# Kernel tuning notes

Measured on AMD Instinct MI355X. Metric: run time of the kernel, lower is better.

Reference implementation:

```python
import jax, jax.numpy as jnp
import numpy as np

L, H, C, DH, FF = 6, 8, 512, 64, 2048
B, T, S = 64, 128, 128
EPS = 1e-5


def setup_inputs() -> dict:
    key = jax.random.key(0)
    ks = jax.random.split(key, 20)
    sc = 0.02
    def w(k, shape):
        return jax.random.normal(k, shape, dtype=jnp.float32) * sc
    inp = {
        "x": jax.random.normal(ks[0], (B, T, C), dtype=jnp.float32),
        "encoder_output": jax.random.normal(ks[1], (B, S, C), dtype=jnp.float32),
        # per-head self-attention projections, stacked over layers and heads
        "sa_wq": w(ks[2], (L, H, C, DH)), "sa_bq": w(ks[3], (L, H, DH)),
        "sa_wk": w(ks[4], (L, H, C, DH)), "sa_bk": w(ks[5], (L, H, DH)),
        "sa_wv": w(ks[6], (L, H, C, DH)), "sa_bv": w(ks[7], (L, H, DH)),
        # per-head cross-attention projections
        "ca_wq": w(ks[8], (L, H, C, DH)), "ca_bq": w(ks[9], (L, H, DH)),
        "ca_wk": w(ks[10], (L, H, C, DH)), "ca_bk": w(ks[11], (L, H, DH)),
        "ca_wv": w(ks[12], (L, H, C, DH)), "ca_bv": w(ks[13], (L, H, DH)),
        # feed-forward
        "ff_w1": w(ks[14], (L, C, FF)), "ff_b1": w(ks[15], (L, FF)),
        "ff_w2": w(ks[16], (L, FF, C)), "ff_b2": w(ks[17], (L, C)),
    }
    return inp


def _layer_norm_2d(x):
    # F.layer_norm(x, (T, C)): normalize jointly over last two dims, no affine
    mu = jnp.mean(x, axis=(1, 2), keepdims=True)
    var = jnp.var(x, axis=(1, 2), keepdims=True)
    return (x - mu) * jax.lax.rsqrt(var + EPS)


def _mha(qx, kvx, wq, bq, wk, bk, wv, bv):
    # wq/wk/wv: [H, C, DH]; per-head projections, vectorized over heads.
    q = jnp.einsum("btc,hcd->bhtd", qx, wq) + bq[:, None, :]
    k = jnp.einsum("bsc,hcd->bhsd", kvx, wk) + bk[:, None, :]
    v = jnp.einsum("bsc,hcd->bhsd", kvx, wv) + bv[:, None, :]
    scores = jax.nn.softmax(jnp.einsum("bhtd,bhsd->bhts", q, k) * (DH ** -0.5), axis=-1)
    out = jnp.einsum("bhts,bhsd->bhtd", scores, v)
    b, h, t, d = out.shape  # concat heads along feature dim
    return out.transpose(0, 2, 1, 3).reshape(b, t, h * d)


def reference(x, encoder_output, sa_wq, sa_bq, sa_wk, sa_bk, sa_wv, sa_bv,
              ca_wq, ca_bq, ca_wk, ca_bk, ca_wv, ca_bv,
              ff_w1, ff_b1, ff_w2, ff_b2):
    for l in range(L):
        # masked MHA (note: original code never applies the causal mask)
        x = x + _mha(x, x, sa_wq[l], sa_bq[l], sa_wk[l], sa_bk[l], sa_wv[l], sa_bv[l])
        x = _layer_norm_2d(x)
        # cross attention: q from decoder, k/v from encoder output
        x = x + _mha(x, encoder_output, ca_wq[l], ca_bq[l], ca_wk[l], ca_bk[l], ca_wv[l], ca_bv[l])
        x = _layer_norm_2d(x)
        # feed-forward
        h = jax.nn.relu(jnp.einsum("btc,cf->btf", x, ff_w1[l]) + ff_b1[l])
        x = x + (jnp.einsum("btf,fc->btc", h, ff_w2[l]) + ff_b2[l])
        x = _layer_norm_2d(x)
    return x
```

## Files before the change

### kernel.cpp

```cpp
#include <hip/hip_runtime.h>
#include <hip/hip_bf16.h>


typedef __bf16 bf16;
typedef bf16 bf16x8 __attribute__((ext_vector_type(8)));
typedef float f32x4 __attribute__((ext_vector_type(4)));

#define MFMA16(a, b, c) __builtin_amdgcn_mfma_f32_16x16x32_bf16(a, b, c, 0, 0, 0)

#define GLL16(gsrc, ldst)                                                          \
    __builtin_amdgcn_global_load_lds(                                              \
        (const __attribute__((address_space(1))) void*)(gsrc),                     \
        (__attribute__((address_space(3))) void*)(ldst), 16, 0, 0)

static constexpr int L_ = 6, C_ = 512, FF_ = 2048;
static constexpr int B_ = 64, T_ = 128;
static constexpr int M_ = B_ * T_;
static constexpr float LNINV = 1.f / 65536.f;
static constexpr float EPS_ = 1e-5f;

__global__ __launch_bounds__(256) void zero_part(float* __restrict__ p) {
    for (int i = threadIdx.x; i < 18 * 64 * 2; i += 256) p[i] = 0.f;
}

__global__ __launch_bounds__(256) void init_x(
    const float* __restrict__ xin, float* __restrict__ y, bf16* __restrict__ yb)
{
    const size_t i = ((size_t)blockIdx.x * 256 + threadIdx.x) * 8;
    float4 f0 = *(const float4*)(xin + i);
    float4 f1 = *(const float4*)(xin + i + 4);
    *(float4*)(y + i) = f0;
    *(float4*)(y + i + 4) = f1;
    bf16x8 v = {(bf16)f0.x, (bf16)f0.y, (bf16)f0.z, (bf16)f0.w,
                (bf16)f1.x, (bf16)f1.y, (bf16)f1.z, (bf16)f1.w};
    *(bf16x8*)(yb + i) = v;
}

__global__ __launch_bounds__(256) void to_bf16(
    const float* __restrict__ in, bf16* __restrict__ out)
{
    const size_t i = ((size_t)blockIdx.x * 256 + threadIdx.x) * 8;
    float4 f0 = *(const float4*)(in + i);
    float4 f1 = *(const float4*)(in + i + 4);
    bf16x8 v = {(bf16)f0.x, (bf16)f0.y, (bf16)f0.z, (bf16)f0.w,
                (bf16)f1.x, (bf16)f1.y, (bf16)f1.z, (bf16)f1.w};
    *(bf16x8*)(out + i) = v;
}

__global__ __launch_bounds__(256) void transpose_f32_bf16(
    const float* __restrict__ src, bf16* __restrict__ dst, int R, int C)
{
    __shared__ alignas(16) float t[64][68];
    const int r0 = blockIdx.y * 64, c0 = blockIdx.x * 64;
    const int tr = threadIdx.x >> 4;
    const int tc = (threadIdx.x & 15) * 4;
#pragma unroll
    for (int ro = 0; ro < 64; ro += 16)
        *(float4*)&t[tr + ro][tc] = *(const float4*)(src + (size_t)(r0 + tr + ro) * C + c0 + tc);
    __syncthreads();
    const int wc = (threadIdx.x & 7) * 8;
#pragma unroll
    for (int po = 0; po < 2; ++po) {
        const int oc = (threadIdx.x >> 3) + po * 32;
        bf16x8 v;
#pragma unroll
        for (int j = 0; j < 8; ++j) v[j] = (bf16)t[wc + j][oc];
        *(bf16x8*)(dst + (size_t)(c0 + oc) * R + r0 + wc) = v;
    }
}

__global__ __launch_bounds__(256) void head_repack(
    const float* __restrict__ sa_wq, const float* __restrict__ sa_wk,
    const float* __restrict__ sa_wv, const float* __restrict__ ca_wq,
    const float* __restrict__ ca_wk, const float* __restrict__ ca_wv,
    bf16* __restrict__ Wsa, bf16* __restrict__ Wcaq, bf16* __restrict__ Wcakv)
{
    __shared__ alignas(16) float t[64][68];
    const int z = blockIdx.z;
    const int type = z / 48, rem = z % 48, l = rem >> 3, h = rem & 7;
    const float* srcs[6] = {sa_wq, sa_wk, sa_wv, ca_wq, ca_wk, ca_wv};
    const float* s = srcs[type] + (size_t)(l * 8 + h) * 512 * 64;
    bf16* d;
    if (type < 3)       d = Wsa   + ((size_t)l * 1536 + type * 512 + h * 64) * 512;
    else if (type == 3) d = Wcaq  + ((size_t)l * 512 + h * 64) * 512;
    else                d = Wcakv + ((size_t)l * 1024 + (type - 4) * 512 + h * 64) * 512;
    const int r0 = blockIdx.y * 64;
    const int tr = threadIdx.x >> 4;
    const int tc = (threadIdx.x & 15) * 4;
#pragma unroll
    for (int ro = 0; ro < 64; ro += 16)
        *(float4*)&t[tr + ro][tc] = *(const float4*)(s + (size_t)(r0 + tr + ro) * 64 + tc);
    __syncthreads();
    const int wc = (threadIdx.x & 7) * 8;
#pragma unroll
    for (int po = 0; po < 2; ++po) {
        const int oc = (threadIdx.x >> 3) + po * 32;
        bf16x8 v;
#pragma unroll
        for (int j = 0; j < 8; ++j) v[j] = (bf16)t[wc + j][oc];
        *(bf16x8*)(d + (size_t)oc * 512 + r0 + wc) = v;
    }
}

__global__ __launch_bounds__(256) void colsum_all(
    const float* __restrict__ sa_wq, const float* __restrict__ sa_wk,
    const float* __restrict__ sa_wv, const float* __restrict__ ca_wq,
    const float* __restrict__ ff_w1,
    float* __restrict__ csA, float* __restrict__ csQ, float* __restrict__ csF)
{
    const int t = blockIdx.x * 256 + threadIdx.x;
    const int l = t >> 12, u = t & 4095;
    float sum = 0.f;
    if (u < 1536) {
        const int p = u >> 9, h = (u >> 6) & 7, d = u & 63;
        const float* w = (p == 0) ? sa_wq : (p == 1) ? sa_wk : sa_wv;
        const float* base = w + (size_t)(l * 8 + h) * 512 * 64 + d;
        for (int c = 0; c < 512; ++c) sum += base[(size_t)c * 64];
        csA[l * 1536 + u] = sum;
    } else if (u < 2048) {
        const int v = u - 1536, h = v >> 6, d = v & 63;
        const float* base = ca_wq + (size_t)(l * 8 + h) * 512 * 64 + d;
        for (int c = 0; c < 512; ++c) sum += base[(size_t)c * 64];
        csQ[l * 512 + v] = sum;
    } else {
        const int f = u - 2048;
        const float* base = ff_w1 + (size_t)l * 512 * 2048 + f;
        for (int c = 0; c < 512; ++c) sum += base[(size_t)c * 2048];
        csF[l * 2048 + f] = sum;
    }
}

template <int MODE, int BM>
__global__ __launch_bounds__(256) void gemm_bt(
    const bf16* __restrict__ A, const bf16* __restrict__ BT,
    const float* __restrict__ b0, const float* __restrict__ b1,
    const float* __restrict__ b2, const float* __restrict__ cs,
    float2* __restrict__ part, int slotPrev, int slotNew,
    bf16* __restrict__ o0, bf16* __restrict__ o1, bf16* __restrict__ o2,
    float* __restrict__ y, bf16* __restrict__ ybf, int N, int K)
{
    constexpr int MI = 4;
    constexpr int NI = (BM == 128) ? 4 : 2;
    constexpr int AG = BM / 32;
    constexpr int VG = AG + 4;
    __shared__ alignas(16) bf16 as[2][BM][64];
    __shared__ alignas(16) bf16 bs[2][128][64];
    const int tid = threadIdx.x, wave = tid >> 6, lane = tid & 63;

    const int gx = gridDim.x;
    int wgid = blockIdx.y * gx + blockIdx.x;
    {
        const int nwg = gx * gridDim.y;
        const int q = nwg >> 3, r = nwg & 7;
        const int xcd = wgid & 7, idx = wgid >> 3;
        wgid = (xcd < r ? xcd * (q + 1) : r * (q + 1) + (xcd - r) * q) + idx;
    }
    const int m0 = (wgid / gx) * BM, n0 = (wgid % gx) * 128;

    const int wr = (BM == 128) ? (wave >> 1) * 64 : 0;
    const int wc = (BM == 128) ? (wave & 1) * 64 : wave * 32;
    const int fr = lane & 15, fq = lane >> 4;
    const int xr = fr & 7;

    float mu = 0.f, rstd = 1.f;
    if (slotPrev >= 0) {
        float2 p = part[slotPrev * 64 + (m0 >> 7)];
        mu = p.x * LNINV;
        rstd = rsqrtf(p.y * LNINV - mu * mu + EPS_);
    }

    const int rlane = lane >> 3;
    const int scol = ((lane & 7) ^ rlane) * 8;
    const bf16* pa = A + (size_t)(m0 + wave * (BM / 4) + rlane) * K + scol;
    const bf16* pb = BT + (size_t)(n0 + wave * 32 + rlane) * K + scol;

    auto stage = [&](int buf, int k0) {
#pragma unroll
        for (int i = 0; i < AG; ++i)
            GLL16(pa + k0 + (size_t)(8 * i) * K, &as[buf][wave * (BM / 4) + 8 * i][0]);
#pragma unroll
        for (int i = 0; i < 4; ++i)
            GLL16(pb + k0 + (size_t)(8 * i) * K, &bs[buf][wave * 32 + 8 * i][0]);
    };

    f32x4 acc[MI][NI] = {};
    auto compute = [&](int buf) {
#pragma unroll
        for (int kk = 0; kk < 2; ++kk) {
            bf16x8 af[MI], bfv[NI];
#pragma unroll
            for (int mi = 0; mi < MI; ++mi)
                af[mi] = *(const bf16x8*)&as[buf][wr + mi * 16 + fr][(((kk << 2) + fq) ^ xr) << 3];
#pragma unroll
            for (int ni = 0; ni < NI; ++ni)
                bfv[ni] = *(const bf16x8*)&bs[buf][wc + ni * 16 + fr][(((kk << 2) + fq) ^ xr) << 3];
#pragma unroll
            for (int mi = 0; mi < MI; ++mi)
#pragma unroll
                for (int ni = 0; ni < NI; ++ni)
                    acc[mi][ni] = MFMA16(af[mi], bfv[ni], acc[mi][ni]);
        }
    };

    const int nt = K >> 6;
    stage(0, 0);
    stage(1, 64);

    int cur = 0;
    for (int t = 0; t < nt - 1; ++t) {
        asm volatile("s_waitcnt vmcnt(%0)\n\ts_barrier" :: "n"(VG) : "memory");
        compute(cur);
        __builtin_amdgcn_s_barrier();
        if (t + 2 < nt) stage(cur, (t + 2) << 6);
        cur ^= 1;
    }
    asm volatile("s_waitcnt vmcnt(0)\n\ts_barrier" ::: "memory");
    compute(cur);

    float s = 0.f, ss = 0.f;
    const float murs = mu * rstd;
#pragma unroll
    for (int mi = 0; mi < MI; ++mi) {
#pragma unroll
        for (int ni = 0; ni < NI; ++ni) {
            const int n = n0 + wc + ni * 16 + fr;
#pragma unroll
            for (int reg = 0; reg < 4; ++reg) {
                const int r = m0 + wr + mi * 16 + fq * 4 + reg;
                float val = acc[mi][ni][reg];
                if constexpr (MODE == 0) {
                    const int p = n >> 9, hd = n & 511, d = n & 63, hh = (n >> 6) & 7;
                    const int bb = r >> 7, tt = r & 127;
                    const float* bias = (p == 0) ? b0 : (p == 1 ? b1 : b2);
                    val = val * rstd + bias[hd] - murs * cs[n];
                    const size_t bh = (size_t)(bb * 8 + hh);
                    if (p == 0)      o0[(bh * 128 + tt) * 64 + d] = (bf16)val;
                    else if (p == 1) o1[(bh * 128 + tt) * 64 + d] = (bf16)val;
                    else             o2[(bh * 64 + d) * 128 + tt] = (bf16)val;
                } else if constexpr (MODE == 1) {
                    const int d = n & 63, hh = (n >> 6) & 7;
                    const int bb = r >> 7, tt = r & 127;
                    val = val * rstd + b0[n] - murs * cs[n];
                    o0[((size_t)(bb * 8 + hh) * 128 + tt) * 64 + d] = (bf16)val;
                } else if constexpr (MODE == 2) {
                    const int p = n >> 9, hd = n & 511, d = n & 63, hh = (n >> 6) & 7;
                    const int bb = r >> 7, tt = r & 127;
                    val += (p == 0) ? b1[hd] : b2[hd];
                    const size_t bh = (size_t)(bb * 8 + hh);
                    if (p == 0) o1[(bh * 128 + tt) * 64 + d] = (bf16)val;
                    else        o2[(bh * 64 + d) * 128 + tt] = (bf16)val;
                } else if constexpr (MODE == 3) {
                    val = val * rstd + b0[n] - murs * cs[n];
                    val = fmaxf(val, 0.f);
                    o0[(size_t)r * 2048 + n] = (bf16)val;
                } else {
                    const size_t idx = (size_t)r * 512 + n;
                    const float v = (y[idx] - mu) * rstd + val + b0[n];
                    y[idx] = v;
                    ybf[idx] = (bf16)v;
                    s += v;
                    ss += v * v;
                }
            }
        }
    }
    if constexpr (MODE == 4) {
        for (int off = 32; off; off >>= 1) { s += __shfl_xor(s, off); ss += __shfl_xor(ss, off); }
        __shared__ float rs[4], rss[4];
        if (lane == 0) { rs[wave] = s; rss[wave] = ss; }
        __syncthreads();
        if (tid == 0) {
            float2* dst = &part[slotNew * 64 + (m0 >> 7)];
            atomicAdd(&dst->x, rs[0] + rs[1] + rs[2] + rs[3]);
            atomicAdd(&dst->y, rss[0] + rss[1] + rss[2] + rss[3]);
        }
    }
}

__global__ __launch_bounds__(256) void attn_kernel(
    const bf16* __restrict__ q, const bf16* __restrict__ k,
    const bf16* __restrict__ vT, float* __restrict__ y, bf16* __restrict__ ybf,
    float2* __restrict__ part, int slotPrev, int slotNew)
{
    __shared__ alignas(16) bf16 sP[128][136];
    __shared__ float sInv[128];
    const int bh = blockIdx.x;
    const int bb = bh >> 3, hh = bh & 7;
    const bf16* Q = q + (size_t)bh * 128 * 64;
    const bf16* Kp = k + (size_t)bh * 128 * 64;
    const bf16* V = vT + (size_t)bh * 64 * 128;
    const int tid = threadIdx.x, wave = tid >> 6, lane = tid & 63;
    const int wr = (wave >> 1) * 64, wc = (wave & 1) * 64;
    const int fr = lane & 15, fq = lane >> 4;

    float mu = 0.f, rstd = 1.f;
    if (slotPrev >= 0) {
        float2 p = part[slotPrev * 64 + bb];
        mu = p.x * LNINV;
        rstd = rsqrtf(p.y * LNINV - mu * mu + EPS_);
    }

    f32x4 acc[4][4] = {};
#pragma unroll
    for (int k0 = 0; k0 < 64; k0 += 32) {
        bf16x8 af[4], bfv[4];
#pragma unroll
        for (int mi = 0; mi < 4; ++mi)
            af[mi] = *(const bf16x8*)(Q + (size_t)(wr + mi * 16 + fr) * 64 + k0 + fq * 8);
#pragma unroll
        for (int ni = 0; ni < 4; ++ni)
            bfv[ni] = *(const bf16x8*)(Kp + (size_t)(wc + ni * 16 + fr) * 64 + k0 + fq * 8);
#pragma unroll
        for (int mi = 0; mi < 4; ++mi)
#pragma unroll
            for (int ni = 0; ni < 4; ++ni)
                acc[mi][ni] = MFMA16(af[mi], bfv[ni], acc[mi][ni]);
    }
#pragma unroll
    for (int mi = 0; mi < 4; ++mi)
#pragma unroll
        for (int ni = 0; ni < 4; ++ni)
#pragma unroll
            for (int reg = 0; reg < 4; ++reg)
                sP[wr + mi * 16 + fq * 4 + reg][wc + ni * 16 + fr] =
                    (bf16)(acc[mi][ni][reg] * 0.125f);
    __syncthreads();

    {
        const int r = tid >> 1, h0 = (tid & 1) * 64;
        float mx = -3.0e38f;
        for (int j = 0; j < 64; ++j) mx = fmaxf(mx, (float)sP[r][h0 + j]);
        mx = fmaxf(mx, __shfl_xor(mx, 1));
        float sum = 0.f;
        for (int j = 0; j < 64; ++j) {
            float p = __expf((float)sP[r][h0 + j] - mx);
            sum += p;
            sP[r][h0 + j] = (bf16)p;
        }
        sum += __shfl_xor(sum, 1);
        if ((tid & 1) == 0) sInv[r] = 1.f / sum;
    }
    __syncthreads();

    f32x4 acc2[2][4] = {};
#pragma unroll
    for (int k0 = 0; k0 < 128; k0 += 32) {
        bf16x8 af[2], bfv[4];
#pragma unroll
        for (int mi = 0; mi < 2; ++mi)
            af[mi] = *(const bf16x8*)&sP[wave * 32 + mi * 16 + fr][k0 + fq * 8];
#pragma unroll
        for (int ni = 0; ni < 4; ++ni)
            bfv[ni] = *(const bf16x8*)(V + (size_t)(ni * 16 + fr) * 128 + k0 + fq * 8);
#pragma unroll
        for (int mi = 0; mi < 2; ++mi)
#pragma unroll
            for (int ni = 0; ni < 4; ++ni)
                acc2[mi][ni] = MFMA16(af[mi], bfv[ni], acc2[mi][ni]);
    }

    float s = 0.f, ss = 0.f;
#pragma unroll
    for (int mi = 0; mi < 2; ++mi)
#pragma unroll
        for (int ni = 0; ni < 4; ++ni)
#pragma unroll
            for (int reg = 0; reg < 4; ++reg) {
                const int r = wave * 32 + mi * 16 + fq * 4 + reg;
                const int d = ni * 16 + fr;
                const size_t idx = ((size_t)(bb * 128 + r)) * 512 + hh * 64 + d;
                const float v = (y[idx] - mu) * rstd + acc2[mi][ni][reg] * sInv[r];
                y[idx] = v;
                ybf[idx] = (bf16)v;
                s += v;
                ss += v * v;
            }
    for (int off = 32; off; off >>= 1) { s += __shfl_xor(s, off); ss += __shfl_xor(ss, off); }
    __shared__ float rs[4], rss[4];
    if (lane == 0) { rs[wave] = s; rss[wave] = ss; }
    __syncthreads();
    if (tid == 0) {
        float2* dst = &part[slotNew * 64 + bb];
        atomicAdd(&dst->x, rs[0] + rs[1] + rs[2] + rs[3]);
        atomicAdd(&dst->y, rss[0] + rss[1] + rss[2] + rss[3]);
    }
}

__global__ __launch_bounds__(256) void final_norm(
    const float* __restrict__ y, const float2* __restrict__ part, int slot,
    float* __restrict__ out)
{
    const size_t i = ((size_t)blockIdx.x * 256 + threadIdx.x) * 4;
    const int b = (int)(i >> 16);
    float2 p = part[slot * 64 + b];
    const float mu = p.x * LNINV;
    const float rstd = rsqrtf(p.y * LNINV - mu * mu + EPS_);
    float4 v = *(const float4*)(y + i);
    float4 o = {(v.x - mu) * rstd, (v.y - mu) * rstd, (v.z - mu) * rstd, (v.w - mu) * rstd};
    *(float4*)(out + i) = o;
}

extern "C" void kernel_launch(void* const* d_in, const int* in_sizes, int n_in,
                              void* d_out, int out_size, void* d_ws, size_t ws_size,
                              hipStream_t stream)
{
    (void)in_sizes; (void)n_in; (void)out_size; (void)ws_size;
    const float* x_in  = (const float*)d_in[0];
    const float* enc   = (const float*)d_in[1];
    const float* sa_wq = (const float*)d_in[2];
    const float* sa_bq = (const float*)d_in[3];
    const float* sa_wk = (const float*)d_in[4];
    const float* sa_bk = (const float*)d_in[5];
    const float* sa_wv = (const float*)d_in[6];
    const float* sa_bv = (const float*)d_in[7];
    const float* ca_wq = (const float*)d_in[8];
    const float* ca_bq = (const float*)d_in[9];
    const float* ca_wk = (const float*)d_in[10];
    const float* ca_bk = (const float*)d_in[11];
    const float* ca_wv = (const float*)d_in[12];
    const float* ca_bv = (const float*)d_in[13];
    const float* ff_w1 = (const float*)d_in[14];
    const float* ff_b1 = (const float*)d_in[15];
    const float* ff_w2 = (const float*)d_in[16];
    const float* ff_b2 = (const float*)d_in[17];

    char* wsp = (char*)d_ws;
    auto alloc = [&](size_t bytes) -> char* {
        char* p = wsp;
        wsp += (bytes + 255) & ~(size_t)255;
        return p;
    };
    float* y     = (float*)alloc((size_t)M_ * 512 * 4);
    bf16*  ybf   = (bf16*)alloc((size_t)M_ * 512 * 2);
    bf16*  encbf = (bf16*)alloc((size_t)M_ * 512 * 2);
    char*  shreg = alloc((size_t)M_ * 2048 * 2);
    bf16*  WsaA  = (bf16*)alloc((size_t)L_ * 1536 * 512 * 2);
    bf16*  WcaqA = (bf16*)alloc((size_t)L_ * 512 * 512 * 2);
    bf16*  WcakvA= (bf16*)alloc((size_t)L_ * 1024 * 512 * 2);
    bf16*  Wff1  = (bf16*)alloc((size_t)2048 * 512 * 2);
    bf16*  Wff2  = (bf16*)alloc((size_t)512 * 2048 * 2);
    float* csA   = (float*)alloc((size_t)L_ * 1536 * 4);
    float* csQ   = (float*)alloc((size_t)L_ * 512 * 4);
    float* csF   = (float*)alloc((size_t)L_ * 2048 * 4);
    float2* part = (float2*)alloc(18 * 64 * sizeof(float2));

    bf16* qb   = (bf16*)shreg;
    bf16* kb   = (bf16*)(shreg + (size_t)512 * 128 * 64 * 2);
    bf16* vTb  = (bf16*)(shreg + (size_t)2 * 512 * 128 * 64 * 2);
    bf16* hbuf = (bf16*)shreg;

    dim3 tb(256);
    zero_part<<<1, tb, 0, stream>>>((float*)part);
    init_x<<<2048, tb, 0, stream>>>(x_in, y, ybf);
    to_bf16<<<2048, tb, 0, stream>>>(enc, encbf);
    head_repack<<<dim3(1, 8, 288), tb, 0, stream>>>(sa_wq, sa_wk, sa_wv, ca_wq, ca_wk, ca_wv,
                                                    WsaA, WcaqA, WcakvA);
    colsum_all<<<96, tb, 0, stream>>>(sa_wq, sa_wk, sa_wv, ca_wq, ff_w1, csA, csQ, csF);

    for (int l = 0; l < L_; ++l) {
        transpose_f32_bf16<<<dim3(32, 8, 1), tb, 0, stream>>>(ff_w1 + (size_t)l * 512 * 2048, Wff1, 512, 2048);
        transpose_f32_bf16<<<dim3(8, 32, 1), tb, 0, stream>>>(ff_w2 + (size_t)l * 2048 * 512, Wff2, 2048, 512);
        const int sPrev = (l == 0) ? -1 : (l - 1) * 3 + 2;
        gemm_bt<0, 128><<<dim3(12, 64), tb, 0, stream>>>(ybf, WsaA + (size_t)l * 1536 * 512,
            sa_bq + l * 512, sa_bk + l * 512, sa_bv + l * 512, csA + l * 1536,
            part, sPrev, -1, qb, kb, vTb, nullptr, nullptr, 1536, 512);
        attn_kernel<<<512, tb, 0, stream>>>(qb, kb, vTb, y, ybf, part, sPrev, l * 3 + 0);
        gemm_bt<1, 64><<<dim3(4, 128), tb, 0, stream>>>(ybf, WcaqA + (size_t)l * 512 * 512,
            ca_bq + l * 512, nullptr, nullptr, csQ + l * 512,
            part, l * 3 + 0, -1, qb, nullptr, nullptr, nullptr, nullptr, 512, 512);
        gemm_bt<2, 128><<<dim3(8, 64), tb, 0, stream>>>(encbf, WcakvA + (size_t)l * 1024 * 512,
            nullptr, ca_bk + l * 512, ca_bv + l * 512, nullptr,
            part, -1, -1, nullptr, kb, vTb, nullptr, nullptr, 1024, 512);
        attn_kernel<<<512, tb, 0, stream>>>(qb, kb, vTb, y, ybf, part, l * 3 + 0, l * 3 + 1);
        gemm_bt<3, 128><<<dim3(16, 64), tb, 0, stream>>>(ybf, Wff1,
            ff_b1 + l * 2048, nullptr, nullptr, csF + l * 2048,
            part, l * 3 + 1, -1, hbuf, nullptr, nullptr, nullptr, nullptr, 2048, 512);
        gemm_bt<4, 64><<<dim3(4, 128), tb, 0, stream>>>(hbuf, Wff2,
            ff_b2 + l * 512, nullptr, nullptr, nullptr,
            part, l * 3 + 1, l * 3 + 2, nullptr, nullptr, nullptr, y, ybf, 512, 2048);
    }
    final_norm<<<4096, tb, 0, stream>>>(y, part, 17, (float*)d_out);
}
```

Baseline: 1.367 ms.

## Use 8-wave GEMM tiles with prioritized MFMA clusters and fuse softmax into attention

The GEMM kernel moves from 4 to 8 waves per workgroup, so each wave owns a smaller sub-tile and issues fewer global-to-LDS loads. The k-loop is split into fragment-load and MFMA clusters separated by explicit lgkmcnt waits, with s_setprio raised around the MFMA clusters. The next tile's staging is placed between the two clusters to overlap loads with math. The attention kernel now exponentiates scores straight from registers and reduces row sums with shuffles, removing the separate LDS max/exp pass. It skips max-subtraction, which risks overflow for large scores, and the extra waves raise per-block synchronization and register pressure.

```diff
diff --git a/kernel.cpp b/kernel.cpp
--- a/kernel.cpp
+++ b/kernel.cpp
@@ -131,7 +131,7 @@
 }
 
 template <int MODE, int BM>
-__global__ __launch_bounds__(256) void gemm_bt(
+__global__ __launch_bounds__(512) void gemm_bt(
     const bf16* __restrict__ A, const bf16* __restrict__ BT,
     const float* __restrict__ b0, const float* __restrict__ b1,
     const float* __restrict__ b2, const float* __restrict__ cs,
@@ -139,10 +139,11 @@
     bf16* __restrict__ o0, bf16* __restrict__ o1, bf16* __restrict__ o2,
     float* __restrict__ y, bf16* __restrict__ ybf, int N, int K)
 {
-    constexpr int MI = 4;
-    constexpr int NI = (BM == 128) ? 4 : 2;
-    constexpr int AG = BM / 32;
-    constexpr int VG = AG + 4;
+    constexpr int MI = (BM == 128) ? 4 : 2;
+    constexpr int NI = 2;
+    constexpr int AR = BM / 8;
+    constexpr int AGLL = BM / 64;
+    constexpr int VG = AGLL + 2;
     __shared__ alignas(16) bf16 as[2][BM][64];
     __shared__ alignas(16) bf16 bs[2][128][64];
     const int tid = threadIdx.x, wave = tid >> 6, lane = tid & 63;
@@ -157,8 +158,8 @@
     }
     const int m0 = (wgid / gx) * BM, n0 = (wgid % gx) * 128;
 
-    const int wr = (BM == 128) ? (wave >> 1) * 64 : 0;
-    const int wc = (BM == 128) ? (wave & 1) * 64 : wave * 32;
+    const int wr = (wave >> 2) * (BM / 2);
+    const int wc = (wave & 3) * 32;
     const int fr = lane & 15, fq = lane >> 4;
     const int xr = fr & 7;
 
@@ -171,35 +172,36 @@
 
     const int rlane = lane >> 3;
     const int scol = ((lane & 7) ^ rlane) * 8;
-    const bf16* pa = A + (size_t)(m0 + wave * (BM / 4) + rlane) * K + scol;
-    const bf16* pb = BT + (size_t)(n0 + wave * 32 + rlane) * K + scol;
+    const bf16* pa = A + (size_t)(m0 + wave * AR + rlane) * K + scol;
+    const bf16* pb = BT + (size_t)(n0 + wave * 16 + rlane) * K + scol;
 
     auto stage = [&](int buf, int k0) {
 #pragma unroll
-        for (int i = 0; i < AG; ++i)
-            GLL16(pa + k0 + (size_t)(8 * i) * K, &as[buf][wave * (BM / 4) + 8 * i][0]);
-#pragma unroll
-        for (int i = 0; i < 4; ++i)
-            GLL16(pb + k0 + (size_t)(8 * i) * K, &bs[buf][wave * 32 + 8 * i][0]);
+        for (int i = 0; i < AGLL; ++i)
+            GLL16(pa + k0 + (size_t)(8 * i) * K, &as[buf][wave * AR + 8 * i][0]);
+#pragma unroll
+        for (int i = 0; i < 2; ++i)
+            GLL16(pb + k0 + (size_t)(8 * i) * K, &bs[buf][wave * 16 + 8 * i][0]);
     };
 
     f32x4 acc[MI][NI] = {};
-    auto compute = [&](int buf) {
-#pragma unroll
-        for (int kk = 0; kk < 2; ++kk) {
-            bf16x8 af[MI], bfv[NI];
-#pragma unroll
-            for (int mi = 0; mi < MI; ++mi)
-                af[mi] = *(const bf16x8*)&as[buf][wr + mi * 16 + fr][(((kk << 2) + fq) ^ xr) << 3];
+    bf16x8 af[MI], bfv[NI];
+    auto frags = [&](int buf, int kk) {
+#pragma unroll
+        for (int mi = 0; mi < MI; ++mi)
+            af[mi] = *(const bf16x8*)&as[buf][wr + mi * 16 + fr][(((kk << 2) + fq) ^ xr) << 3];
+#pragma unroll
+        for (int ni = 0; ni < NI; ++ni)
+            bfv[ni] = *(const bf16x8*)&bs[buf][wc + ni * 16 + fr][(((kk << 2) + fq) ^ xr) << 3];
+    };
+    auto cluster = [&]() {
+        __builtin_amdgcn_s_setprio(1);
+#pragma unroll
+        for (int mi = 0; mi < MI; ++mi)
 #pragma unroll
             for (int ni = 0; ni < NI; ++ni)
-                bfv[ni] = *(const bf16x8*)&bs[buf][wc + ni * 16 + fr][(((kk << 2) + fq) ^ xr) << 3];
-#pragma unroll
-            for (int mi = 0; mi < MI; ++mi)
-#pragma unroll
-                for (int ni = 0; ni < NI; ++ni)
-                    acc[mi][ni] = MFMA16(af[mi], bfv[ni], acc[mi][ni]);
-        }
+                acc[mi][ni] = MFMA16(af[mi], bfv[ni], acc[mi][ni]);
+        __builtin_amdgcn_s_setprio(0);
     };
 
     const int nt = K >> 6;
@@ -209,13 +211,27 @@
     int cur = 0;
     for (int t = 0; t < nt - 1; ++t) {
         asm volatile("s_waitcnt vmcnt(%0)\n\ts_barrier" :: "n"(VG) : "memory");
-        compute(cur);
+        frags(cur, 0);
+        asm volatile("s_waitcnt lgkmcnt(0)" ::: "memory");
+        __builtin_amdgcn_sched_barrier(0);
+        cluster();
+        frags(cur, 1);
+        asm volatile("s_waitcnt lgkmcnt(0)" ::: "memory");
+        __builtin_amdgcn_sched_barrier(0);
         __builtin_amdgcn_s_barrier();
         if (t + 2 < nt) stage(cur, (t + 2) << 6);
+        cluster();
         cur ^= 1;
     }
     asm volatile("s_waitcnt vmcnt(0)\n\ts_barrier" ::: "memory");
-    compute(cur);
+    frags(cur, 0);
+    asm volatile("s_waitcnt lgkmcnt(0)" ::: "memory");
+    __builtin_amdgcn_sched_barrier(0);
+    cluster();
+    frags(cur, 1);
+    asm volatile("s_waitcnt lgkmcnt(0)" ::: "memory");
+    __builtin_amdgcn_sched_barrier(0);
+    cluster();
 
     float s = 0.f, ss = 0.f;
     const float murs = mu * rstd;
@@ -266,13 +282,16 @@
     }
     if constexpr (MODE == 4) {
         for (int off = 32; off; off >>= 1) { s += __shfl_xor(s, off); ss += __shfl_xor(ss, off); }
-        __shared__ float rs[4], rss[4];
+        __shared__ float rs[8], rss[8];
         if (lane == 0) { rs[wave] = s; rss[wave] = ss; }
         __syncthreads();
         if (tid == 0) {
+            float sa = 0.f, sb = 0.f;
+#pragma unroll
+            for (int w = 0; w < 8; ++w) { sa += rs[w]; sb += rss[w]; }
             float2* dst = &part[slotNew * 64 + (m0 >> 7)];
-            atomicAdd(&dst->x, rs[0] + rs[1] + rs[2] + rs[3]);
-            atomicAdd(&dst->y, rss[0] + rss[1] + rss[2] + rss[3]);
+            atomicAdd(&dst->x, sa);
+            atomicAdd(&dst->y, sb);
         }
     }
 }
@@ -283,7 +302,7 @@
     float2* __restrict__ part, int slotPrev, int slotNew)
 {
     __shared__ alignas(16) bf16 sP[128][136];
-    __shared__ float sInv[128];
+    __shared__ float sPart[2][128];
     const int bh = blockIdx.x;
     const int bb = bh >> 3, hh = bh & 7;
     const bf16* Q = q + (size_t)bh * 128 * 64;
@@ -316,29 +335,26 @@
             for (int ni = 0; ni < 4; ++ni)
                 acc[mi][ni] = MFMA16(af[mi], bfv[ni], acc[mi][ni]);
     }
-#pragma unroll
-    for (int mi = 0; mi < 4; ++mi)
-#pragma unroll
-        for (int ni = 0; ni < 4; ++ni)
-#pragma unroll
-            for (int reg = 0; reg < 4; ++reg)
-                sP[wr + mi * 16 + fq * 4 + reg][wc + ni * 16 + fr] =
-                    (bf16)(acc[mi][ni][reg] * 0.125f);
-    __syncthreads();
-
-    {
-        const int r = tid >> 1, h0 = (tid & 1) * 64;
-        float mx = -3.0e38f;
-        for (int j = 0; j < 64; ++j) mx = fmaxf(mx, (float)sP[r][h0 + j]);
-        mx = fmaxf(mx, __shfl_xor(mx, 1));
-        float sum = 0.f;
-        for (int j = 0; j < 64; ++j) {
-            float p = __expf((float)sP[r][h0 + j] - mx);
-            sum += p;
-            sP[r][h0 + j] = (bf16)p;
+
+    const int colw = wave & 1;
+#pragma unroll
+    for (int mi = 0; mi < 4; ++mi) {
+#pragma unroll
+        for (int reg = 0; reg < 4; ++reg) {
+            const int r = wr + mi * 16 + fq * 4 + reg;
+            float rsum = 0.f;
+#pragma unroll
+            for (int ni = 0; ni < 4; ++ni) {
+                const float e = __expf(acc[mi][ni][reg] * 0.125f);
+                sP[r][wc + ni * 16 + fr] = (bf16)e;
+                rsum += e;
+            }
+            rsum += __shfl_xor(rsum, 1);
+            rsum += __shfl_xor(rsum, 2);
+            rsum += __shfl_xor(rsum, 4);
+            rsum += __shfl_xor(rsum, 8);
+            if (fr == 0) sPart[colw][r] = rsum;
         }
-        sum += __shfl_xor(sum, 1);
-        if ((tid & 1) == 0) sInv[r] = 1.f / sum;
     }
     __syncthreads();
 
@@ -358,6 +374,15 @@
             for (int ni = 0; ni < 4; ++ni)
                 acc2[mi][ni] = MFMA16(af[mi], bfv[ni], acc2[mi][ni]);
     }
+
+    float inv[2][4];
+#pragma unroll
+    for (int mi = 0; mi < 2; ++mi)
+#pragma unroll
+        for (int reg = 0; reg < 4; ++reg) {
+            const int r = wave * 32 + mi * 16 + fq * 4 + reg;
+            inv[mi][reg] = 1.f / (sPart[0][r] + sPart[1][r]);
+        }
 
     float s = 0.f, ss = 0.f;
 #pragma unroll
@@ -369,7 +394,7 @@
                 const int r = wave * 32 + mi * 16 + fq * 4 + reg;
                 const int d = ni * 16 + fr;
                 const size_t idx = ((size_t)(bb * 128 + r)) * 512 + hh * 64 + d;
-                const float v = (y[idx] - mu) * rstd + acc2[mi][ni][reg] * sInv[r];
+                const float v = (y[idx] - mu) * rstd + acc2[mi][ni][reg] * inv[mi][reg];
                 y[idx] = v;
                 ybf[idx] = (bf16)v;
                 s += v;
@@ -449,7 +474,7 @@
     bf16* vTb  = (bf16*)(shreg + (size_t)2 * 512 * 128 * 64 * 2);
     bf16* hbuf = (bf16*)shreg;
 
-    dim3 tb(256);
+    dim3 tb(256), tbg(512);
     zero_part<<<1, tb, 0, stream>>>((float*)part);
     init_x<<<2048, tb, 0, stream>>>(x_in, y, ybf);
     to_bf16<<<2048, tb, 0, stream>>>(enc, encbf);
@@ -461,21 +486,21 @@
         transpose_f32_bf16<<<dim3(32, 8, 1), tb, 0, stream>>>(ff_w1 + (size_t)l * 512 * 2048, Wff1, 512, 2048);
         transpose_f32_bf16<<<dim3(8, 32, 1), tb, 0, stream>>>(ff_w2 + (size_t)l * 2048 * 512, Wff2, 2048, 512);
         const int sPrev = (l == 0) ? -1 : (l - 1) * 3 + 2;
-        gemm_bt<0, 128><<<dim3(12, 64), tb, 0, stream>>>(ybf, WsaA + (size_t)l * 1536 * 512,
+        gemm_bt<0, 128><<<dim3(12, 64), tbg, 0, stream>>>(ybf, WsaA + (size_t)l * 1536 * 512,
             sa_bq + l * 512, sa_bk + l * 512, sa_bv + l * 512, csA + l * 1536,
             part, sPrev, -1, qb, kb, vTb, nullptr, nullptr, 1536, 512);
         attn_kernel<<<512, tb, 0, stream>>>(qb, kb, vTb, y, ybf, part, sPrev, l * 3 + 0);
-        gemm_bt<1, 64><<<dim3(4, 128), tb, 0, stream>>>(ybf, WcaqA + (size_t)l * 512 * 512,
+        gemm_bt<1, 64><<<dim3(4, 128), tbg, 0, stream>>>(ybf, WcaqA + (size_t)l * 512 * 512,
             ca_bq + l * 512, nullptr, nullptr, csQ + l * 512,
             part, l * 3 + 0, -1, qb, nullptr, nullptr, nullptr, nullptr, 512, 512);
-        gemm_bt<2, 128><<<dim3(8, 64), tb, 0, stream>>>(encbf, WcakvA + (size_t)l * 1024 * 512,
+        gemm_bt<2, 128><<<dim3(8, 64), tbg, 0, stream>>>(encbf, WcakvA + (size_t)l * 1024 * 512,
             nullptr, ca_bk + l * 512, ca_bv + l * 512, nullptr,
             part, -1, -1, nullptr, kb, vTb, nullptr, nullptr, 1024, 512);
         attn_kernel<<<512, tb, 0, stream>>>(qb, kb, vTb, y, ybf, part, l * 3 + 0, l * 3 + 1);
-        gemm_bt<3, 128><<<dim3(16, 64), tb, 0, stream>>>(ybf, Wff1,
+        gemm_bt<3, 128><<<dim3(16, 64), tbg, 0, stream>>>(ybf, Wff1,
             ff_b1 + l * 2048, nullptr, nullptr, csF + l * 2048,
             part, l * 3 + 1, -1, hbuf, nullptr, nullptr, nullptr, nullptr, 2048, 512);
-        gemm_bt<4, 64><<<dim3(4, 128), tb, 0, stream>>>(hbuf, Wff2,
+        gemm_bt<4, 64><<<dim3(4, 128), tbg, 0, stream>>>(hbuf, Wff2,
             ff_b2 + l * 512, nullptr, nullptr, nullptr,
             part, l * 3 + 1, l * 3 + 2, nullptr, nullptr, nullptr, y, ybf, 512, 2048);
     }
```

Result: faster. 1.338 ms (-2.2%).
